# Performance work log

Hardware: AMD Instinct MI355X
Metric: run time of the kernel (lower is better)

## Reference

```python
import jax, jax.numpy as jnp
import numpy as np

N_NODES = 50000
N_EDGES = 800000
IN_F = 128
H_F = 128
OUT_F = 128
N_GRAPHS = 128


def setup_inputs() -> dict:
    key = jax.random.key(0)
    ks = jax.random.split(key, 7)
    x = jax.random.normal(ks[0], (N_NODES, IN_F), dtype=jnp.float32)
    edge_index = jax.random.randint(ks[1], (2, N_EDGES), 0, N_NODES, dtype=jnp.int32)
    batch = jnp.sort(jax.random.randint(ks[2], (N_NODES,), 0, N_GRAPHS, dtype=jnp.int32))
    s1 = 1.0 / np.sqrt(IN_F)
    s2 = 1.0 / np.sqrt(H_F)
    W1 = jax.random.uniform(ks[3], (IN_F, H_F), jnp.float32, -s1, s1)
    b1 = jnp.zeros((H_F,), jnp.float32)
    W2 = jax.random.uniform(ks[4], (H_F, OUT_F), jnp.float32, -s2, s2)
    b2 = jnp.zeros((OUT_F,), jnp.float32)
    return {"x": x, "edge_index": edge_index, "batch": batch,
            "W1": W1, "b1": b1, "W2": W2, "b2": b2}


def _gcn_conv(x, W, b, src, dst, n_nodes):
    # PyG GCNConv: out = D^{-1/2} (A + I) D^{-1/2} (x W) + b
    h = x @ W  # [N, out]
    # degree including self-loop
    deg = jax.ops.segment_sum(jnp.ones_like(dst, dtype=h.dtype), dst,
                              num_segments=n_nodes) + 1.0
    dinv = jax.lax.rsqrt(deg)  # [N]
    norm = dinv[src] * dinv[dst]  # [E]
    agg = jax.ops.segment_sum(h[src] * norm[:, None], dst, num_segments=n_nodes)
    # self-loop term has norm dinv[i]^2
    return agg + (dinv * dinv)[:, None] * h + b


def reference(x, edge_index, batch, W1, b1, W2, b2):
    src, dst = edge_index[0], edge_index[1]
    h = jax.nn.relu(_gcn_conv(x, W1, b1, src, dst, N_NODES))
    h = _gcn_conv(h, W2, b2, src, dst, N_NODES)
    # global_add_pool over graphs
    return jax.ops.segment_sum(h, batch, num_segments=N_GRAPHS)
```

## Files before the change

### kernel.cpp

```cpp
#include <hip/hip_runtime.h>
#include <hip/hip_bf16.h>


typedef _Float16 f16x8 __attribute__((ext_vector_type(8)));
typedef float f32x4 __attribute__((ext_vector_type(4)));

#define BCHUNK 4096

static __device__ __forceinline__ float f16lo(unsigned int u) {
    union { unsigned short s; _Float16 h; } c; c.s = (unsigned short)(u & 0xffff);
    return (float)c.h;
}
static __device__ __forceinline__ float f16hi(unsigned int u) {
    union { unsigned short s; _Float16 h; } c; c.s = (unsigned short)(u >> 16);
    return (float)c.h;
}
static __device__ __forceinline__ unsigned int pack2f16(float x, float y) {
    union { unsigned short s; _Float16 h; } a, b;
    a.h = (_Float16)x; b.h = (_Float16)y;
    return (unsigned int)a.s | ((unsigned int)b.s << 16);
}


__global__ __launch_bounds__(256) void bin_hist(const int* __restrict__ ei,
                                                int* __restrict__ counts,
                                                int E, int NB, int NBLK) {
    __shared__ int hist[256];
    int t = threadIdx.x, blk = blockIdx.x;
    for (int b = t; b < NB; b += 256) hist[b] = 0;
    __syncthreads();
    int base = blk * BCHUNK;
    int end = min(E, base + BCHUNK);
    for (int e = base + t; e < end; e += 256)
        atomicAdd(&hist[ei[E + e] >> 8], 1);
    __syncthreads();
    for (int b = t; b < NB; b += 256) counts[b * NBLK + blk] = hist[b];
}

__global__ __launch_bounds__(256) void bin_scatter(const int* __restrict__ ei,
                                                   const int* __restrict__ counts,
                                                   unsigned int* __restrict__ bedges,
                                                   int E, int NB, int NBLK) {
    __shared__ int lcur[256];
    int t = threadIdx.x, blk = blockIdx.x;
    for (int b = t; b < NB; b += 256) lcur[b] = counts[b * NBLK + blk];
    __syncthreads();
    int base = blk * BCHUNK;
    int end = min(E, base + BCHUNK);
    for (int e = base + t; e < end; e += 256) {
        int s = ei[e];
        int d = ei[E + e];
        int pos = atomicAdd(&lcur[d >> 8], 1);
        bedges[pos] = (unsigned int)s | ((unsigned int)(d & 255) << 16);
    }
}

__global__ __launch_bounds__(256) void deg_buckets(const unsigned int* __restrict__ bedges,
                                                   const int* __restrict__ counts,
                                                   int* __restrict__ cnt,
                                                   int E, int N, int NB, int NBLK) {
    __shared__ int lcnt[256];
    int b = blockIdx.x, t = threadIdx.x;
    lcnt[t] = 0;
    __syncthreads();
    int bstart = counts[b * NBLK];
    int bend = (b + 1 < NB) ? counts[(b + 1) * NBLK] : E;
    for (int i = bstart + t; i < bend; i += 256)
        atomicAdd(&lcnt[bedges[i] >> 16], 1);
    __syncthreads();
    int node = (b << 8) + t;
    if (node < N) cnt[node] = lcnt[t];
}

__global__ __launch_bounds__(256) void fill_buckets(const unsigned int* __restrict__ bedges,
                                                    const int* __restrict__ counts,
                                                    const int* __restrict__ row_start,
                                                    int* __restrict__ srcs,
                                                    int E, int N, int NB, int NBLK) {
    __shared__ int lcur[256];
    int b = blockIdx.x, t = threadIdx.x;
    int node = (b << 8) + t;
    lcur[t] = (node < N) ? row_start[node] : 0;
    __syncthreads();
    int bstart = counts[b * NBLK];
    int bend = (b + 1 < NB) ? counts[(b + 1) * NBLK] : E;
    for (int i = bstart + t; i < bend; i += 256) {
        unsigned int p = bedges[i];
        int pos = atomicAdd(&lcur[p >> 16], 1);
        srcs[pos] = (int)(p & 0xffffu);
    }
}


__global__ void block_sums(const int* __restrict__ data, int* __restrict__ bsum, int n) {
    __shared__ int s[256];
    int base = blockIdx.x * 1024;
    int t = threadIdx.x;
    int v = 0;
#pragma unroll
    for (int i = 0; i < 4; i++) {
        int idx = base + t * 4 + i;
        if (idx < n) v += data[idx];
    }
    s[t] = v;
    __syncthreads();
    for (int off = 128; off > 0; off >>= 1) {
        if (t < off) s[t] += s[t + off];
        __syncthreads();
    }
    if (t == 0) bsum[blockIdx.x] = s[0];
}

__global__ void scan_bsum(int* __restrict__ bsum, int nb) {
    int lane = threadIdx.x & 63;
    int v = (lane < nb) ? bsum[lane] : 0;
    int incl = v;
#pragma unroll
    for (int off = 1; off < 64; off *= 2) {
        int u = __shfl_up(incl, off);
        if (lane >= off) incl += u;
    }
    if (lane < nb) bsum[lane] = incl - v;
}

__global__ void scan_apply(int* __restrict__ data, const int* __restrict__ bsum, int n) {
    __shared__ int s[256];
    int base = blockIdx.x * 1024;
    int t = threadIdx.x;
    int loc[4];
    int v = 0;
#pragma unroll
    for (int i = 0; i < 4; i++) {
        int idx = base + t * 4 + i;
        loc[i] = (idx < n) ? data[idx] : 0;
        v += loc[i];
    }
    s[t] = v;
    __syncthreads();
    for (int off = 1; off < 256; off *= 2) {
        int u = (t >= off) ? s[t - off] : 0;
        __syncthreads();
        s[t] += u;
        __syncthreads();
    }
    int excl = s[t] - v + bsum[blockIdx.x];
#pragma unroll
    for (int i = 0; i < 4; i++) {
        int idx = base + t * 4 + i;
        if (idx < n) { data[idx] = excl; excl += loc[i]; }
    }
}

__global__ void scan_nodes(const int* __restrict__ cnt, const int* __restrict__ bsum,
                           int* __restrict__ row_start, float* __restrict__ dinv, int n) {
    __shared__ int s[256];
    int base = blockIdx.x * 1024;
    int t = threadIdx.x;
    int loc[4];
    int v = 0;
#pragma unroll
    for (int i = 0; i < 4; i++) {
        int idx = base + t * 4 + i;
        loc[i] = (idx < n) ? cnt[idx] : 0;
        v += loc[i];
    }
    s[t] = v;
    __syncthreads();
    for (int off = 1; off < 256; off *= 2) {
        int u = (t >= off) ? s[t - off] : 0;
        __syncthreads();
        s[t] += u;
        __syncthreads();
    }
    int excl = s[t] - v + bsum[blockIdx.x];
#pragma unroll
    for (int i = 0; i < 4; i++) {
        int idx = base + t * 4 + i;
        if (idx < n) {
            row_start[idx] = excl;
            dinv[idx] = rsqrtf((float)loc[i] + 1.0f);
            excl += loc[i];
        }
    }
}

__global__ void wprep(const float* __restrict__ W, _Float16* __restrict__ wfrag) {
    int idx = blockIdx.x * 256 + threadIdx.x;
    if (idx >= 2048) return;
    int lane = idx & 63;
    int kc = (idx >> 6) & 3;
    int nb = idx >> 8;
    int col = nb * 16 + (lane & 15);
    int krow = kc * 32 + (lane >> 4) * 8;
#pragma unroll
    for (int j = 0; j < 8; j++)
        wfrag[idx * 8 + j] = (_Float16)W[(krow + j) * 128 + col];
}

__global__ __launch_bounds__(256) void gemm_mfma_f32in(const float* __restrict__ A,
                                                       const _Float16* __restrict__ wfrag,
                                                       _Float16* __restrict__ C, int M) {
    __shared__ _Float16 As[128 * 136];
    int t = threadIdx.x;
    int row0 = blockIdx.x * 128;

    const float4* A4 = (const float4*)A;
#pragma unroll
    for (int it = 0; it < 16; it++) {
        int v = it * 256 + t;
        int row = v >> 5;
        int seg = v & 31;
        float4 val = make_float4(0.f, 0.f, 0.f, 0.f);
        if (row0 + row < M) val = A4[(size_t)(row0 + row) * 32 + seg];
        _Float16* p = &As[row * 136 + seg * 4];
        p[0] = (_Float16)val.x; p[1] = (_Float16)val.y;
        p[2] = (_Float16)val.z; p[3] = (_Float16)val.w;
    }
    __syncthreads();

    int wv = t >> 6;
    int lane = t & 63;
    int lrow = lane & 15;
    int lq = lane >> 4;

    f32x4 acc[2][8];
#pragma unroll
    for (int i = 0; i < 2; i++)
#pragma unroll
        for (int j = 0; j < 8; j++) acc[i][j] = (f32x4){0.f, 0.f, 0.f, 0.f};

#pragma unroll
    for (int kc = 0; kc < 4; kc++) {
        int k0 = kc * 32;
        f16x8 a0 = *((const f16x8*)&As[(wv * 32 + lrow) * 136 + k0 + lq * 8]);
        f16x8 a1 = *((const f16x8*)&As[(wv * 32 + 16 + lrow) * 136 + k0 + lq * 8]);
#pragma unroll
        for (int nb = 0; nb < 8; nb++) {
            f16x8 b = ((const f16x8*)wfrag)[(nb * 4 + kc) * 64 + lane];
            acc[0][nb] = __builtin_amdgcn_mfma_f32_16x16x32_f16(a0, b, acc[0][nb], 0, 0, 0);
            acc[1][nb] = __builtin_amdgcn_mfma_f32_16x16x32_f16(a1, b, acc[1][nb], 0, 0, 0);
        }
    }

#pragma unroll
    for (int ti = 0; ti < 2; ti++) {
#pragma unroll
        for (int r = 0; r < 4; r++) {
            int row = row0 + wv * 32 + ti * 16 + lq * 4 + r;
            if (row < M) {
#pragma unroll
                for (int nb = 0; nb < 8; nb++)
                    C[(size_t)row * 128 + nb * 16 + lrow] = (_Float16)acc[ti][nb][r];
            }
        }
    }
}

__global__ __launch_bounds__(256) void agg1(const _Float16* __restrict__ hb,
                                            const int* __restrict__ srcs,
                                            const int* __restrict__ row_start,
                                            const int* __restrict__ cnt,
                                            const float* __restrict__ dinv,
                                            const float* __restrict__ bias,
                                            _Float16* __restrict__ ob, int n) {
    int node = blockIdx.x * 4 + (threadIdx.x >> 6);
    if (node >= n) return;
    int lane = threadIdx.x & 63;
    int s0 = row_start[node];
    int c = cnt[node];
    float dn = dinv[node];
    const unsigned int* h2 = (const unsigned int*)hb;
    float ax = 0.f, ay = 0.f, bx = 0.f, by = 0.f;
    int e = 0;
    for (; e + 8 <= c; e += 8) {
        int s0i = srcs[s0 + e + 0];
        int s1i = srcs[s0 + e + 1];
        int s2i = srcs[s0 + e + 2];
        int s3i = srcs[s0 + e + 3];
        int s4i = srcs[s0 + e + 4];
        int s5i = srcs[s0 + e + 5];
        int s6i = srcs[s0 + e + 6];
        int s7i = srcs[s0 + e + 7];
        float d0 = dinv[s0i], d1 = dinv[s1i], d2 = dinv[s2i], d3 = dinv[s3i];
        float d4 = dinv[s4i], d5 = dinv[s5i], d6 = dinv[s6i], d7 = dinv[s7i];
        unsigned int v0 = h2[(size_t)s0i * 64 + lane];
        unsigned int v1 = h2[(size_t)s1i * 64 + lane];
        unsigned int v2 = h2[(size_t)s2i * 64 + lane];
        unsigned int v3 = h2[(size_t)s3i * 64 + lane];
        unsigned int v4 = h2[(size_t)s4i * 64 + lane];
        unsigned int v5 = h2[(size_t)s5i * 64 + lane];
        unsigned int v6 = h2[(size_t)s6i * 64 + lane];
        unsigned int v7 = h2[(size_t)s7i * 64 + lane];
        float w0 = d0 * dn, w1 = d1 * dn, w2 = d2 * dn, w3 = d3 * dn;
        float w4 = d4 * dn, w5 = d5 * dn, w6 = d6 * dn, w7 = d7 * dn;
        ax = fmaf(w0, f16lo(v0), ax); ay = fmaf(w0, f16hi(v0), ay);
        bx = fmaf(w1, f16lo(v1), bx); by = fmaf(w1, f16hi(v1), by);
        ax = fmaf(w2, f16lo(v2), ax); ay = fmaf(w2, f16hi(v2), ay);
        bx = fmaf(w3, f16lo(v3), bx); by = fmaf(w3, f16hi(v3), by);
        ax = fmaf(w4, f16lo(v4), ax); ay = fmaf(w4, f16hi(v4), ay);
        bx = fmaf(w5, f16lo(v5), bx); by = fmaf(w5, f16hi(v5), by);
        ax = fmaf(w6, f16lo(v6), ax); ay = fmaf(w6, f16hi(v6), ay);
        bx = fmaf(w7, f16lo(v7), bx); by = fmaf(w7, f16hi(v7), by);
    }
    for (; e + 4 <= c; e += 4) {
        int s0i = srcs[s0 + e + 0];
        int s1i = srcs[s0 + e + 1];
        int s2i = srcs[s0 + e + 2];
        int s3i = srcs[s0 + e + 3];
        float d0 = dinv[s0i], d1 = dinv[s1i], d2 = dinv[s2i], d3 = dinv[s3i];
        unsigned int v0 = h2[(size_t)s0i * 64 + lane];
        unsigned int v1 = h2[(size_t)s1i * 64 + lane];
        unsigned int v2 = h2[(size_t)s2i * 64 + lane];
        unsigned int v3 = h2[(size_t)s3i * 64 + lane];
        float w0 = d0 * dn, w1 = d1 * dn, w2 = d2 * dn, w3 = d3 * dn;
        ax = fmaf(w0, f16lo(v0), ax); ay = fmaf(w0, f16hi(v0), ay);
        bx = fmaf(w1, f16lo(v1), bx); by = fmaf(w1, f16hi(v1), by);
        ax = fmaf(w2, f16lo(v2), ax); ay = fmaf(w2, f16hi(v2), ay);
        bx = fmaf(w3, f16lo(v3), bx); by = fmaf(w3, f16hi(v3), by);
    }
    for (; e < c; e++) {
        int si = srcs[s0 + e];
        float w = dinv[si] * dn;
        unsigned int v = h2[(size_t)si * 64 + lane];
        ax = fmaf(w, f16lo(v), ax); ay = fmaf(w, f16hi(v), ay);
    }
    ax += bx; ay += by;
    float sw = dn * dn;
    unsigned int hs = h2[(size_t)node * 64 + lane];
    float2 bv = ((const float2*)bias)[lane];
    float ox = ax + sw * f16lo(hs) + bv.x;
    float oy = ay + sw * f16hi(hs) + bv.y;
    ox = fmaxf(ox, 0.f); oy = fmaxf(oy, 0.f);
    ((unsigned int*)ob)[(size_t)node * 64 + lane] = pack2f16(ox, oy);
}

__global__ __launch_bounds__(256) void agg2_pool(const _Float16* __restrict__ ob,
                                                 const int* __restrict__ srcs,
                                                 const int* __restrict__ row_start,
                                                 const int* __restrict__ cnt,
                                                 const float* __restrict__ dinv,
                                                 const int* __restrict__ batch,
                                                 float* __restrict__ P, int n) {
    __shared__ float red[4][128];
    int wv = threadIdx.x >> 6;
    int lane = threadIdx.x & 63;
    int base = blockIdx.x * 4;
    int node = base + wv;
    const unsigned int* h2 = (const unsigned int*)ob;
    float ax = 0.f, ay = 0.f, bx = 0.f, by = 0.f;
    int g = -1;
    if (node < n) {
        g = batch[node];
        int s0 = row_start[node];
        int c = cnt[node];
        float dn = dinv[node];
        int e = 0;
        for (; e + 8 <= c; e += 8) {
            int s0i = srcs[s0 + e + 0];
            int s1i = srcs[s0 + e + 1];
            int s2i = srcs[s0 + e + 2];
            int s3i = srcs[s0 + e + 3];
            int s4i = srcs[s0 + e + 4];
            int s5i = srcs[s0 + e + 5];
            int s6i = srcs[s0 + e + 6];
            int s7i = srcs[s0 + e + 7];
            float d0 = dinv[s0i], d1 = dinv[s1i], d2 = dinv[s2i], d3 = dinv[s3i];
            float d4 = dinv[s4i], d5 = dinv[s5i], d6 = dinv[s6i], d7 = dinv[s7i];
            unsigned int v0 = h2[(size_t)s0i * 64 + lane];
            unsigned int v1 = h2[(size_t)s1i * 64 + lane];
            unsigned int v2 = h2[(size_t)s2i * 64 + lane];
            unsigned int v3 = h2[(size_t)s3i * 64 + lane];
            unsigned int v4 = h2[(size_t)s4i * 64 + lane];
            unsigned int v5 = h2[(size_t)s5i * 64 + lane];
            unsigned int v6 = h2[(size_t)s6i * 64 + lane];
            unsigned int v7 = h2[(size_t)s7i * 64 + lane];
            float w0 = d0 * dn, w1 = d1 * dn, w2 = d2 * dn, w3 = d3 * dn;
            float w4 = d4 * dn, w5 = d5 * dn, w6 = d6 * dn, w7 = d7 * dn;
            ax = fmaf(w0, f16lo(v0), ax); ay = fmaf(w0, f16hi(v0), ay);
            bx = fmaf(w1, f16lo(v1), bx); by = fmaf(w1, f16hi(v1), by);
            ax = fmaf(w2, f16lo(v2), ax); ay = fmaf(w2, f16hi(v2), ay);
            bx = fmaf(w3, f16lo(v3), bx); by = fmaf(w3, f16hi(v3), by);
            ax = fmaf(w4, f16lo(v4), ax); ay = fmaf(w4, f16hi(v4), ay);
            bx = fmaf(w5, f16lo(v5), bx); by = fmaf(w5, f16hi(v5), by);
            ax = fmaf(w6, f16lo(v6), ax); ay = fmaf(w6, f16hi(v6), ay);
            bx = fmaf(w7, f16lo(v7), bx); by = fmaf(w7, f16hi(v7), by);
        }
        for (; e + 4 <= c; e += 4) {
            int s0i = srcs[s0 + e + 0];
            int s1i = srcs[s0 + e + 1];
            int s2i = srcs[s0 + e + 2];
            int s3i = srcs[s0 + e + 3];
            float d0 = dinv[s0i], d1 = dinv[s1i], d2 = dinv[s2i], d3 = dinv[s3i];
            unsigned int v0 = h2[(size_t)s0i * 64 + lane];
            unsigned int v1 = h2[(size_t)s1i * 64 + lane];
            unsigned int v2 = h2[(size_t)s2i * 64 + lane];
            unsigned int v3 = h2[(size_t)s3i * 64 + lane];
            float w0 = d0 * dn, w1 = d1 * dn, w2 = d2 * dn, w3 = d3 * dn;
            ax = fmaf(w0, f16lo(v0), ax); ay = fmaf(w0, f16hi(v0), ay);
            bx = fmaf(w1, f16lo(v1), bx); by = fmaf(w1, f16hi(v1), by);
            ax = fmaf(w2, f16lo(v2), ax); ay = fmaf(w2, f16hi(v2), ay);
            bx = fmaf(w3, f16lo(v3), bx); by = fmaf(w3, f16hi(v3), by);
        }
        for (; e < c; e++) {
            int si = srcs[s0 + e];
            float w = dinv[si] * dn;
            unsigned int v = h2[(size_t)si * 64 + lane];
            ax = fmaf(w, f16lo(v), ax); ay = fmaf(w, f16hi(v), ay);
        }
        ax += bx; ay += by;
        float sw = dn * dn;
        unsigned int hs = h2[(size_t)node * 64 + lane];
        ax += sw * f16lo(hs);
        ay += sw * f16hi(hs);
    }
    int lastn = min(base + 3, n - 1);
    bool uniform = (base < n) && (batch[base] == batch[lastn]) && (base + 3 < n);
    if (uniform) {
        red[wv][lane * 2 + 0] = ax;
        red[wv][lane * 2 + 1] = ay;
        __syncthreads();
        if (wv == 0) {
            float sx = red[0][lane * 2] + red[1][lane * 2] + red[2][lane * 2] + red[3][lane * 2];
            float sy = red[0][lane * 2 + 1] + red[1][lane * 2 + 1] + red[2][lane * 2 + 1] + red[3][lane * 2 + 1];
            atomicAdd(&P[g * 128 + lane * 2 + 0], sx);
            atomicAdd(&P[g * 128 + lane * 2 + 1], sy);
        }
    } else if (node < n) {
        atomicAdd(&P[g * 128 + lane * 2 + 0], ax);
        atomicAdd(&P[g * 128 + lane * 2 + 1], ay);
    }
}

__global__ __launch_bounds__(128) void gemm_small(const float* __restrict__ P,
                                                  const float* __restrict__ W2,
                                                  const float* __restrict__ b2,
                                                  const int* __restrict__ batch,
                                                  float* __restrict__ out, int n) {
    __shared__ float prow[128];
    int g = blockIdx.x;
    int c = threadIdx.x;
    prow[c] = P[g * 128 + c];
    __syncthreads();
    int lo = 0, hi = n;
    while (lo < hi) { int mid = (lo + hi) >> 1; if (batch[mid] < g) lo = mid + 1; else hi = mid; }
    int start = lo;
    hi = n;
    while (lo < hi) { int mid = (lo + hi) >> 1; if (batch[mid] < g + 1) lo = mid + 1; else hi = mid; }
    float ng = (float)(lo - start);
    float acc = 0.f;
#pragma unroll 8
    for (int k = 0; k < 128; k++) acc = fmaf(prow[k], W2[k * 128 + c], acc);
    out[g * 128 + c] = acc + ng * b2[c];
}

extern "C" void kernel_launch(void* const* d_in, const int* in_sizes, int n_in,
                              void* d_out, int out_size, void* d_ws, size_t ws_size,
                              hipStream_t stream) {
    const float* x  = (const float*)d_in[0];
    const int*   ei = (const int*)d_in[1];
    const int*   batch = (const int*)d_in[2];
    const float* W1 = (const float*)d_in[3];
    const float* b1 = (const float*)d_in[4];
    const float* W2 = (const float*)d_in[5];
    const float* b2 = (const float*)d_in[6];
    float* out = (float*)d_out;

    const int N = in_sizes[2];
    const int E = in_sizes[1] / 2;

    const int NB = (N + 255) >> 8;
    const int NBLK = (E + BCHUNK - 1) / BCHUNK;
    const int ncounts = NB * NBLK;

    _Float16* hb = (_Float16*)d_ws;
    _Float16* ob = hb + (size_t)N * 128;
    int* cnt  = (int*)(ob + (size_t)N * 128);
    int* row_start = cnt + N;
    float* dinv    = (float*)(row_start + N);
    int* srcs      = (int*)(dinv + N);
    unsigned int* bedges = (unsigned int*)(srcs + E);
    int* counts    = (int*)(bedges + E);
    _Float16* wfrag1 = (_Float16*)(counts + ncounts);
    float* P       = (float*)(wfrag1 + 128 * 128);
    int* bsum      = (int*)(P + 128 * 128);

    const int nbc = (ncounts + 1023) / 1024;
    const int nbn = (N + 1023) / 1024;

    hipMemsetAsync(P, 0, 128 * 128 * sizeof(float), stream);
    wprep<<<8, 256, 0, stream>>>(W1, wfrag1);

    bin_hist<<<NBLK, 256, 0, stream>>>(ei, counts, E, NB, NBLK);
    block_sums<<<nbc, 256, 0, stream>>>(counts, bsum, ncounts);
    scan_bsum<<<1, 64, 0, stream>>>(bsum, nbc);
    scan_apply<<<nbc, 256, 0, stream>>>(counts, bsum, ncounts);
    bin_scatter<<<NBLK, 256, 0, stream>>>(ei, counts, bedges, E, NB, NBLK);
    deg_buckets<<<NB, 256, 0, stream>>>(bedges, counts, cnt, E, N, NB, NBLK);
    block_sums<<<nbn, 256, 0, stream>>>(cnt, bsum, N);
    scan_bsum<<<1, 64, 0, stream>>>(bsum, nbn);
    scan_nodes<<<nbn, 256, 0, stream>>>(cnt, bsum, row_start, dinv, N);
    fill_buckets<<<NB, 256, 0, stream>>>(bedges, counts, row_start, srcs, E, N, NB, NBLK);

    const int gemm_grid = (N + 127) / 128;

    gemm_mfma_f32in<<<gemm_grid, 256, 0, stream>>>(x, wfrag1, hb, N);
    agg1<<<(N + 3) / 4, 256, 0, stream>>>(hb, srcs, row_start, cnt, dinv, b1, ob, N);
    agg2_pool<<<(N + 3) / 4, 256, 0, stream>>>(ob, srcs, row_start, cnt, dinv, batch, P, N);
    gemm_small<<<128, 128, 0, stream>>>(P, W2, b2, batch, out, N);
}
```

Before: 236.4 us.

## Prescale features by dinv and pad CSR rows to 8 with zero sentinel

The GEMM epilogue now multiplies each row by dinv, and agg1 scales its output by dinv as well. This removes the per-edge dinv gathers and multiplies from both aggregation kernels, leaving plain adds. CSR rows are padded to multiples of 8 and filled with a sentinel index pointing at a zeroed extra feature row, so the gather loop can load indices as int4 vectors with a one-step prefetch and needs no remainder loops. The cost is extra gathers of the zero row and a larger srcs buffer, plus some fp16 rounding differences from storing prescaled values.

```diff
diff --git a/kernel.cpp b/kernel.cpp
--- a/kernel.cpp
+++ b/kernel.cpp
@@ -75,6 +75,7 @@
 __global__ __launch_bounds__(256) void fill_buckets(const unsigned int* __restrict__ bedges,
                                                     const int* __restrict__ counts,
                                                     const int* __restrict__ row_start,
+                                                    const int* __restrict__ cnt,
                                                     int* __restrict__ srcs,
                                                     int E, int N, int NB, int NBLK) {
     __shared__ int lcur[256];
@@ -89,6 +90,12 @@
         int pos = atomicAdd(&lcur[p >> 16], 1);
         srcs[pos] = (int)(p & 0xffffu);
     }
+    if (node < N) {
+        int c = cnt[node];
+        int e0 = row_start[node] + c;
+        int e1 = row_start[node] + ((c + 7) & ~7);
+        for (int j = e0; j < e1; j++) srcs[j] = N;
+    }
 }
 
 
@@ -101,6 +108,25 @@
     for (int i = 0; i < 4; i++) {
         int idx = base + t * 4 + i;
         if (idx < n) v += data[idx];
+    }
+    s[t] = v;
+    __syncthreads();
+    for (int off = 128; off > 0; off >>= 1) {
+        if (t < off) s[t] += s[t + off];
+        __syncthreads();
+    }
+    if (t == 0) bsum[blockIdx.x] = s[0];
+}
+
+__global__ void block_sums_pad(const int* __restrict__ data, int* __restrict__ bsum, int n) {
+    __shared__ int s[256];
+    int base = blockIdx.x * 1024;
+    int t = threadIdx.x;
+    int v = 0;
+#pragma unroll
+    for (int i = 0; i < 4; i++) {
+        int idx = base + t * 4 + i;
+        if (idx < n) v += (data[idx] + 7) & ~7;
     }
     s[t] = v;
     __syncthreads();
@@ -156,13 +182,14 @@
     __shared__ int s[256];
     int base = blockIdx.x * 1024;
     int t = threadIdx.x;
-    int loc[4];
+    int loc[4], pc[4];
     int v = 0;
 #pragma unroll
     for (int i = 0; i < 4; i++) {
         int idx = base + t * 4 + i;
         loc[i] = (idx < n) ? cnt[idx] : 0;
-        v += loc[i];
+        pc[i] = (loc[i] + 7) & ~7;
+        v += pc[i];
     }
     s[t] = v;
     __syncthreads();
@@ -179,7 +206,7 @@
         if (idx < n) {
             row_start[idx] = excl;
             dinv[idx] = rsqrtf((float)loc[i] + 1.0f);
-            excl += loc[i];
+            excl += pc[i];
         }
     }
 }
@@ -199,6 +226,7 @@
 
 __global__ __launch_bounds__(256) void gemm_mfma_f32in(const float* __restrict__ A,
                                                        const _Float16* __restrict__ wfrag,
+                                                       const float* __restrict__ dinv,
                                                        _Float16* __restrict__ C, int M) {
     __shared__ _Float16 As[128 * 136];
     int t = threadIdx.x;
@@ -248,9 +276,10 @@
         for (int r = 0; r < 4; r++) {
             int row = row0 + wv * 32 + ti * 16 + lq * 4 + r;
             if (row < M) {
+                float dv = dinv[row];
 #pragma unroll
                 for (int nb = 0; nb < 8; nb++)
-                    C[(size_t)row * 128 + nb * 16 + lrow] = (_Float16)acc[ti][nb][r];
+                    C[(size_t)row * 128 + nb * 16 + lrow] = (_Float16)(acc[ti][nb][r] * dv);
             }
         }
     }
@@ -268,69 +297,40 @@
     int lane = threadIdx.x & 63;
     int s0 = row_start[node];
     int c = cnt[node];
+    int nit = (c + 7) >> 3;
     float dn = dinv[node];
     const unsigned int* h2 = (const unsigned int*)hb;
-    float ax = 0.f, ay = 0.f, bx = 0.f, by = 0.f;
-    int e = 0;
-    for (; e + 8 <= c; e += 8) {
-        int s0i = srcs[s0 + e + 0];
-        int s1i = srcs[s0 + e + 1];
-        int s2i = srcs[s0 + e + 2];
-        int s3i = srcs[s0 + e + 3];
-        int s4i = srcs[s0 + e + 4];
-        int s5i = srcs[s0 + e + 5];
-        int s6i = srcs[s0 + e + 6];
-        int s7i = srcs[s0 + e + 7];
-        float d0 = dinv[s0i], d1 = dinv[s1i], d2 = dinv[s2i], d3 = dinv[s3i];
-        float d4 = dinv[s4i], d5 = dinv[s5i], d6 = dinv[s6i], d7 = dinv[s7i];
-        unsigned int v0 = h2[(size_t)s0i * 64 + lane];
-        unsigned int v1 = h2[(size_t)s1i * 64 + lane];
-        unsigned int v2 = h2[(size_t)s2i * 64 + lane];
-        unsigned int v3 = h2[(size_t)s3i * 64 + lane];
-        unsigned int v4 = h2[(size_t)s4i * 64 + lane];
-        unsigned int v5 = h2[(size_t)s5i * 64 + lane];
-        unsigned int v6 = h2[(size_t)s6i * 64 + lane];
-        unsigned int v7 = h2[(size_t)s7i * 64 + lane];
-        float w0 = d0 * dn, w1 = d1 * dn, w2 = d2 * dn, w3 = d3 * dn;
-        float w4 = d4 * dn, w5 = d5 * dn, w6 = d6 * dn, w7 = d7 * dn;
-        ax = fmaf(w0, f16lo(v0), ax); ay = fmaf(w0, f16hi(v0), ay);
-        bx = fmaf(w1, f16lo(v1), bx); by = fmaf(w1, f16hi(v1), by);
-        ax = fmaf(w2, f16lo(v2), ax); ay = fmaf(w2, f16hi(v2), ay);
-        bx = fmaf(w3, f16lo(v3), bx); by = fmaf(w3, f16hi(v3), by);
-        ax = fmaf(w4, f16lo(v4), ax); ay = fmaf(w4, f16hi(v4), ay);
-        bx = fmaf(w5, f16lo(v5), bx); by = fmaf(w5, f16hi(v5), by);
-        ax = fmaf(w6, f16lo(v6), ax); ay = fmaf(w6, f16hi(v6), ay);
-        bx = fmaf(w7, f16lo(v7), bx); by = fmaf(w7, f16hi(v7), by);
-    }
-    for (; e + 4 <= c; e += 4) {
-        int s0i = srcs[s0 + e + 0];
-        int s1i = srcs[s0 + e + 1];
-        int s2i = srcs[s0 + e + 2];
-        int s3i = srcs[s0 + e + 3];
-        float d0 = dinv[s0i], d1 = dinv[s1i], d2 = dinv[s2i], d3 = dinv[s3i];
-        unsigned int v0 = h2[(size_t)s0i * 64 + lane];
-        unsigned int v1 = h2[(size_t)s1i * 64 + lane];
-        unsigned int v2 = h2[(size_t)s2i * 64 + lane];
-        unsigned int v3 = h2[(size_t)s3i * 64 + lane];
-        float w0 = d0 * dn, w1 = d1 * dn, w2 = d2 * dn, w3 = d3 * dn;
-        ax = fmaf(w0, f16lo(v0), ax); ay = fmaf(w0, f16hi(v0), ay);
-        bx = fmaf(w1, f16lo(v1), bx); by = fmaf(w1, f16hi(v1), by);
-        ax = fmaf(w2, f16lo(v2), ax); ay = fmaf(w2, f16hi(v2), ay);
-        bx = fmaf(w3, f16lo(v3), bx); by = fmaf(w3, f16hi(v3), by);
-    }
-    for (; e < c; e++) {
-        int si = srcs[s0 + e];
-        float w = dinv[si] * dn;
-        unsigned int v = h2[(size_t)si * 64 + lane];
-        ax = fmaf(w, f16lo(v), ax); ay = fmaf(w, f16hi(v), ay);
-    }
-    ax += bx; ay += by;
-    float sw = dn * dn;
     unsigned int hs = h2[(size_t)node * 64 + lane];
     float2 bv = ((const float2*)bias)[lane];
-    float ox = ax + sw * f16lo(hs) + bv.x;
-    float oy = ay + sw * f16hi(hs) + bv.y;
-    ox = fmaxf(ox, 0.f); oy = fmaxf(oy, 0.f);
+    float ax = 0.f, ay = 0.f, bx = 0.f, by = 0.f;
+    const int4* sp = (const int4*)(srcs + s0);
+    int4 sa = {}, sb = {};
+    if (nit > 0) { sa = sp[0]; sb = sp[1]; }
+    for (int it = 0; it < nit; it++) {
+        int4 ca = sa, cb = sb;
+        int nx = (it + 1 < nit) ? it + 1 : it;
+        sa = sp[nx * 2]; sb = sp[nx * 2 + 1];
+        unsigned int v0 = h2[(size_t)(unsigned)ca.x * 64 + lane];
+        unsigned int v1 = h2[(size_t)(unsigned)ca.y * 64 + lane];
+        unsigned int v2 = h2[(size_t)(unsigned)ca.z * 64 + lane];
+        unsigned int v3 = h2[(size_t)(unsigned)ca.w * 64 + lane];
+        unsigned int v4 = h2[(size_t)(unsigned)cb.x * 64 + lane];
+        unsigned int v5 = h2[(size_t)(unsigned)cb.y * 64 + lane];
+        unsigned int v6 = h2[(size_t)(unsigned)cb.z * 64 + lane];
+        unsigned int v7 = h2[(size_t)(unsigned)cb.w * 64 + lane];
+        ax += f16lo(v0); ay += f16hi(v0);
+        bx += f16lo(v1); by += f16hi(v1);
+        ax += f16lo(v2); ay += f16hi(v2);
+        bx += f16lo(v3); by += f16hi(v3);
+        ax += f16lo(v4); ay += f16hi(v4);
+        bx += f16lo(v5); by += f16hi(v5);
+        ax += f16lo(v6); ay += f16hi(v6);
+        bx += f16lo(v7); by += f16hi(v7);
+    }
+    ax += bx + f16lo(hs);
+    ay += by + f16hi(hs);
+    float ox = fmaxf(fmaf(dn, ax, bv.x), 0.f) * dn;
+    float oy = fmaxf(fmaf(dn, ay, bv.y), 0.f) * dn;
     ((unsigned int*)ob)[(size_t)node * 64 + lane] = pack2f16(ox, oy);
 }
 
@@ -347,77 +347,50 @@
     int base = blockIdx.x * 4;
     int node = base + wv;
     const unsigned int* h2 = (const unsigned int*)ob;
-    float ax = 0.f, ay = 0.f, bx = 0.f, by = 0.f;
+    float tx = 0.f, ty = 0.f;
     int g = -1;
     if (node < n) {
         g = batch[node];
         int s0 = row_start[node];
         int c = cnt[node];
+        int nit = (c + 7) >> 3;
         float dn = dinv[node];
-        int e = 0;
-        for (; e + 8 <= c; e += 8) {
-            int s0i = srcs[s0 + e + 0];
-            int s1i = srcs[s0 + e + 1];
-            int s2i = srcs[s0 + e + 2];
-            int s3i = srcs[s0 + e + 3];
-            int s4i = srcs[s0 + e + 4];
-            int s5i = srcs[s0 + e + 5];
-            int s6i = srcs[s0 + e + 6];
-            int s7i = srcs[s0 + e + 7];
-            float d0 = dinv[s0i], d1 = dinv[s1i], d2 = dinv[s2i], d3 = dinv[s3i];
-            float d4 = dinv[s4i], d5 = dinv[s5i], d6 = dinv[s6i], d7 = dinv[s7i];
-            unsigned int v0 = h2[(size_t)s0i * 64 + lane];
-            unsigned int v1 = h2[(size_t)s1i * 64 + lane];
-            unsigned int v2 = h2[(size_t)s2i * 64 + lane];
-            unsigned int v3 = h2[(size_t)s3i * 64 + lane];
-            unsigned int v4 = h2[(size_t)s4i * 64 + lane];
-            unsigned int v5 = h2[(size_t)s5i * 64 + lane];
-            unsigned int v6 = h2[(size_t)s6i * 64 + lane];
-            unsigned int v7 = h2[(size_t)s7i * 64 + lane];
-            float w0 = d0 * dn, w1 = d1 * dn, w2 = d2 * dn, w3 = d3 * dn;
-            float w4 = d4 * dn, w5 = d5 * dn, w6 = d6 * dn, w7 = d7 * dn;
-            ax = fmaf(w0, f16lo(v0), ax); ay = fmaf(w0, f16hi(v0), ay);
-            bx = fmaf(w1, f16lo(v1), bx); by = fmaf(w1, f16hi(v1), by);
-            ax = fmaf(w2, f16lo(v2), ax); ay = fmaf(w2, f16hi(v2), ay);
-            bx = fmaf(w3, f16lo(v3), bx); by = fmaf(w3, f16hi(v3), by);
-            ax = fmaf(w4, f16lo(v4), ax); ay = fmaf(w4, f16hi(v4), ay);
-            bx = fmaf(w5, f16lo(v5), bx); by = fmaf(w5, f16hi(v5), by);
-            ax = fmaf(w6, f16lo(v6), ax); ay = fmaf(w6, f16hi(v6), ay);
-            bx = fmaf(w7, f16lo(v7), bx); by = fmaf(w7, f16hi(v7), by);
+        unsigned int hs = h2[(size_t)node * 64 + lane];
+        float ax = 0.f, ay = 0.f, bx = 0.f, by = 0.f;
+        const int4* sp = (const int4*)(srcs + s0);
+        int4 sa = {}, sb = {};
+        if (nit > 0) { sa = sp[0]; sb = sp[1]; }
+        for (int it = 0; it < nit; it++) {
+            int4 ca = sa, cb = sb;
+            int nx = (it + 1 < nit) ? it + 1 : it;
+            sa = sp[nx * 2]; sb = sp[nx * 2 + 1];
+            unsigned int v0 = h2[(size_t)(unsigned)ca.x * 64 + lane];
+            unsigned int v1 = h2[(size_t)(unsigned)ca.y * 64 + lane];
+            unsigned int v2 = h2[(size_t)(unsigned)ca.z * 64 + lane];
+            unsigned int v3 = h2[(size_t)(unsigned)ca.w * 64 + lane];
+            unsigned int v4 = h2[(size_t)(unsigned)cb.x * 64 + lane];
+            unsigned int v5 = h2[(size_t)(unsigned)cb.y * 64 + lane];
+            unsigned int v6 = h2[(size_t)(unsigned)cb.z * 64 + lane];
+            unsigned int v7 = h2[(size_t)(unsigned)cb.w * 64 + lane];
+            ax += f16lo(v0); ay += f16hi(v0);
+            bx += f16lo(v1); by += f16hi(v1);
+            ax += f16lo(v2); ay += f16hi(v2);
+            bx += f16lo(v3); by += f16hi(v3);
+            ax += f16lo(v4); ay += f16hi(v4);
+            bx += f16lo(v5); by += f16hi(v5);
+            ax += f16lo(v6); ay += f16hi(v6);
+            bx += f16lo(v7); by += f16hi(v7);
         }
-        for (; e + 4 <= c; e += 4) {
-            int s0i = srcs[s0 + e + 0];
-            int s1i = srcs[s0 + e + 1];
-            int s2i = srcs[s0 + e + 2];
-            int s3i = srcs[s0 + e + 3];
-            float d0 = dinv[s0i], d1 = dinv[s1i], d2 = dinv[s2i], d3 = dinv[s3i];
-            unsigned int v0 = h2[(size_t)s0i * 64 + lane];
-            unsigned int v1 = h2[(size_t)s1i * 64 + lane];
-            unsigned int v2 = h2[(size_t)s2i * 64 + lane];
-            unsigned int v3 = h2[(size_t)s3i * 64 + lane];
-            float w0 = d0 * dn, w1 = d1 * dn, w2 = d2 * dn, w3 = d3 * dn;
-            ax = fmaf(w0, f16lo(v0), ax); ay = fmaf(w0, f16hi(v0), ay);
-            bx = fmaf(w1, f16lo(v1), bx); by = fmaf(w1, f16hi(v1), by);
-            ax = fmaf(w2, f16lo(v2), ax); ay = fmaf(w2, f16hi(v2), ay);
-            bx = fmaf(w3, f16lo(v3), bx); by = fmaf(w3, f16hi(v3), by);
-        }
-        for (; e < c; e++) {
-            int si = srcs[s0 + e];
-            float w = dinv[si] * dn;
-            unsigned int v = h2[(size_t)si * 64 + lane];
-            ax = fmaf(w, f16lo(v), ax); ay = fmaf(w, f16hi(v), ay);
-        }
-        ax += bx; ay += by;
-        float sw = dn * dn;
-        unsigned int hs = h2[(size_t)node * 64 + lane];
-        ax += sw * f16lo(hs);
-        ay += sw * f16hi(hs);
+        ax += bx + f16lo(hs);
+        ay += by + f16hi(hs);
+        tx = dn * ax;
+        ty = dn * ay;
     }
     int lastn = min(base + 3, n - 1);
     bool uniform = (base < n) && (batch[base] == batch[lastn]) && (base + 3 < n);
     if (uniform) {
-        red[wv][lane * 2 + 0] = ax;
-        red[wv][lane * 2 + 1] = ay;
+        red[wv][lane * 2 + 0] = tx;
+        red[wv][lane * 2 + 1] = ty;
         __syncthreads();
         if (wv == 0) {
             float sx = red[0][lane * 2] + red[1][lane * 2] + red[2][lane * 2] + red[3][lane * 2];
@@ -426,8 +399,8 @@
             atomicAdd(&P[g * 128 + lane * 2 + 1], sy);
         }
     } else if (node < n) {
-        atomicAdd(&P[g * 128 + lane * 2 + 0], ax);
-        atomicAdd(&P[g * 128 + lane * 2 + 1], ay);
+        atomicAdd(&P[g * 128 + lane * 2 + 0], tx);
+        atomicAdd(&P[g * 128 + lane * 2 + 1], ty);
     }
 }
 
@@ -471,14 +444,15 @@
     const int NB = (N + 255) >> 8;
     const int NBLK = (E + BCHUNK - 1) / BCHUNK;
     const int ncounts = NB * NBLK;
+    const int SRP = E + 7 * N + 16;
 
     _Float16* hb = (_Float16*)d_ws;
-    _Float16* ob = hb + (size_t)N * 128;
-    int* cnt  = (int*)(ob + (size_t)N * 128);
+    _Float16* ob = hb + (size_t)(N + 8) * 128;
+    int* cnt  = (int*)(ob + (size_t)(N + 8) * 128);
     int* row_start = cnt + N;
     float* dinv    = (float*)(row_start + N);
     int* srcs      = (int*)(dinv + N);
-    unsigned int* bedges = (unsigned int*)(srcs + E);
+    unsigned int* bedges = (unsigned int*)(srcs + SRP);
     int* counts    = (int*)(bedges + E);
     _Float16* wfrag1 = (_Float16*)(counts + ncounts);
     float* P       = (float*)(wfrag1 + 128 * 128);
@@ -488,6 +462,8 @@
     const int nbn = (N + 1023) / 1024;
 
     hipMemsetAsync(P, 0, 128 * 128 * sizeof(float), stream);
+    hipMemsetAsync(hb + (size_t)N * 128, 0, 128 * sizeof(_Float16), stream);
+    hipMemsetAsync(ob + (size_t)N * 128, 0, 128 * sizeof(_Float16), stream);
     wprep<<<8, 256, 0, stream>>>(W1, wfrag1);
 
     bin_hist<<<NBLK, 256, 0, stream>>>(ei, counts, E, NB, NBLK);
@@ -496,14 +472,14 @@
     scan_apply<<<nbc, 256, 0, stream>>>(counts, bsum, ncounts);
     bin_scatter<<<NBLK, 256, 0, stream>>>(ei, counts, bedges, E, NB, NBLK);
     deg_buckets<<<NB, 256, 0, stream>>>(bedges, counts, cnt, E, N, NB, NBLK);
-    block_sums<<<nbn, 256, 0, stream>>>(cnt, bsum, N);
+    block_sums_pad<<<nbn, 256, 0, stream>>>(cnt, bsum, N);
     scan_bsum<<<1, 64, 0, stream>>>(bsum, nbn);
     scan_nodes<<<nbn, 256, 0, stream>>>(cnt, bsum, row_start, dinv, N);
-    fill_buckets<<<NB, 256, 0, stream>>>(bedges, counts, row_start, srcs, E, N, NB, NBLK);
+    fill_buckets<<<NB, 256, 0, stream>>>(bedges, counts, row_start, cnt, srcs, E, N, NB, NBLK);
 
     const int gemm_grid = (N + 127) / 128;
 
-    gemm_mfma_f32in<<<gemm_grid, 256, 0, stream>>>(x, wfrag1, hb, N);
+    gemm_mfma_f32in<<<gemm_grid, 256, 0, stream>>>(x, wfrag1, dinv, hb, N);
     agg1<<<(N + 3) / 4, 256, 0, stream>>>(hb, srcs, row_start, cnt, dinv, b1, ob, N);
     agg2_pool<<<(N + 3) / 4, 256, 0, stream>>>(ob, srcs, row_start, cnt, dinv, batch, P, N);
     gemm_small<<<128, 128, 0, stream>>>(P, W2, b2, batch, out, N);
```

Measured after the change: 232.7 us. No clear change (-1.5%).
